# Optimization experiments

Hardware: AMD Instinct MI355X
Metric: run time of the kernel (lower is better)

## Reference

```python
import jax, jax.numpy as jnp
import numpy as np

N = 100000   # num_nodes
D = 128      # hidden_dim
E = 640000   # num_edges


def setup_inputs() -> dict:
    key = jax.random.key(0)
    k0, k1, k2, k3 = jax.random.split(key, 4)
    node_features = jax.random.normal(k0, (N, D), dtype=jnp.float32) * 0.02
    # GCNConv linear weights (glorot-style scale), bias initialized to zero
    scale = 1.0 / np.sqrt(D)
    W1 = jax.random.normal(k1, (D, D), dtype=jnp.float32) * scale
    b1 = jnp.zeros((D,), dtype=jnp.float32)
    W2 = jax.random.normal(k2, (D, D), dtype=jnp.float32) * scale
    b2 = jnp.zeros((D,), dtype=jnp.float32)
    edge_index = jax.random.randint(k3, (2, E), 0, N, dtype=jnp.int32)
    return {"node_features": node_features, "W1": W1, "b1": b1,
            "W2": W2, "b2": b2, "edge_index": edge_index}


def gcn_layer(x, W, b, row, col):
    # PyG GCNConv: linear (no bias) -> symmetric norm deg^-1/2 -> scatter-add -> +bias
    x = x @ W.T                                   # [N, D]
    ones = jnp.ones(row.shape, dtype=x.dtype)
    deg = jax.ops.segment_sum(ones, col, num_segments=N)   # in-degree incl. self-loops
    dis = jnp.where(deg > 0, jax.lax.rsqrt(deg), 0.0)       # deg_inv_sqrt, inf -> 0
    norm = dis[row] * dis[col]                    # [E_tot]
    msgs = norm[:, None] * x[row]                 # gather + scale, [E_tot, D]
    out = jax.ops.segment_sum(msgs, col, num_segments=N)    # scatter-aggregate
    return out + b


def reference(node_features, W1, b1, W2, b2, edge_index):
    # add self-loops once (GCNConv does this per call; same result since graph is static)
    loops = jnp.arange(N, dtype=edge_index.dtype)
    row = jnp.concatenate([edge_index[0], loops])
    col = jnp.concatenate([edge_index[1], loops])
    x = jax.nn.relu(gcn_layer(node_features, W1, b1, row, col))
    x = jax.nn.relu(gcn_layer(x, W2, b2, row, col))
    return x
```

## Files before the change

kernel.cpp:

```cpp
#include <hip/hip_runtime.h>

#define DD 128

typedef short bf16x8 __attribute__((ext_vector_type(8)));
typedef float f32x4 __attribute__((ext_vector_type(4)));

__device__ __forceinline__ unsigned short f2bf(float f) {
    unsigned int u = __builtin_bit_cast(unsigned int, f);
    u += 0x7fffu + ((u >> 16) & 1u);
    return (unsigned short)(u >> 16);
}
__device__ __forceinline__ float bflo(unsigned int u) { return __builtin_bit_cast(float, u << 16); }
__device__ __forceinline__ float bfhi(unsigned int u) { return __builtin_bit_cast(float, u & 0xffff0000u); }

__global__ __launch_bounds__(256) void k_part(const int* __restrict__ cnt,
                                              int* __restrict__ part, int n) {
    __shared__ int s[256];
    int t = threadIdx.x;
    int i = blockIdx.x * 256 + t;
    s[t] = (i < n) ? cnt[i] : 0;
    __syncthreads();
    for (int off = 128; off > 0; off >>= 1) {
        if (t < off) s[t] += s[t + off];
        __syncthreads();
    }
    if (t == 0) part[blockIdx.x] = s[0];
}

__global__ __launch_bounds__(1024) void k_scanpart(int* __restrict__ part, int nblk) {
    __shared__ int s[1024];
    int t = threadIdx.x;
    int v = (t < nblk) ? part[t] : 0;
    s[t] = v;
    __syncthreads();
    for (int off = 1; off < 1024; off <<= 1) {
        int u = (t >= off) ? s[t - off] : 0;
        __syncthreads();
        s[t] += u;
        __syncthreads();
    }
    if (t < nblk) part[t] = s[t] - v;
}

__global__ __launch_bounds__(256) void k_apply(const int* __restrict__ cnt,
                                               const int* __restrict__ part,
                                               int* __restrict__ rowptr,
                                               int* __restrict__ cursor,
                                               float* __restrict__ dis, int n) {
    __shared__ int s[256];
    int t = threadIdx.x;
    int i = blockIdx.x * 256 + t;
    int c = (i < n) ? cnt[i] : 0;
    s[t] = c;
    __syncthreads();
    for (int off = 1; off < 256; off <<= 1) {
        int u = (t >= off) ? s[t - off] : 0;
        __syncthreads();
        s[t] += u;
        __syncthreads();
    }
    int base = part[blockIdx.x] + s[t] - c;
    if (i < n) {
        rowptr[i] = base;
        cursor[i] = base;
        dis[i] = rsqrtf((float)c + 1.0f);
        if (i == n - 1) rowptr[n] = base + c;
    }
}

__global__ void k_permute(const int* __restrict__ row, const int* __restrict__ col,
                          int* __restrict__ cursor, int* __restrict__ srow, int E) {
    int e = blockIdx.x * blockDim.x + threadIdx.x;
    if (e >= E) return;
    int p = atomicAdd(&cursor[col[e]], 1);
    srow[p] = row[e];
}

__global__ __launch_bounds__(512) void k_gemm_mfma(const float* __restrict__ Xv,
                                                   const float* __restrict__ W,
                                                   unsigned short* __restrict__ Y,
                                                   int nrows, int gemm_blocks,
                                                   const int* __restrict__ ecol,
                                                   int* __restrict__ cnt, int E) {
    __shared__ unsigned short Ws[128 * 128];
    const int t = threadIdx.x;

    if ((int)blockIdx.x >= gemm_blocks) {
        int e = (blockIdx.x - gemm_blocks) * 512 + t;
        if (e < E) atomicAdd(&cnt[ecol[e]], 1);
        return;
    }

    #pragma unroll
    for (int i = 0; i < 4; ++i) {
        int g  = i * 512 + t;
        int wr = g >> 4, ch = g & 15;
        const float* src = W + wr * 128 + ch * 8;
        float4 f0 = *(const float4*)src;
        float4 f1 = *(const float4*)(src + 4);
        unsigned short u[8] = { f2bf(f0.x), f2bf(f0.y), f2bf(f0.z), f2bf(f0.w),
                                f2bf(f1.x), f2bf(f1.y), f2bf(f1.z), f2bf(f1.w) };
        int dst = wr * 128 + ((ch ^ (wr & 15)) << 3);
        *(uint4*)&Ws[dst] = *(const uint4*)u;
    }

    const int wid  = t >> 6;
    const int lane = t & 63;
    const int lr   = lane & 15;
    const int lk   = lane >> 4;
    const long base = (long)blockIdx.x * 128;

    long arow = base + wid * 16 + lr;
    bool rowok = arow < nrows;
    if (!rowok) arow = nrows - 1;

    float4 a[8];
    #pragma unroll
    for (int kc = 0; kc < 4; ++kc) {
        const float* ap = Xv + arow * 128 + kc * 32 + lk * 8;
        a[2 * kc]     = *(const float4*)ap;
        a[2 * kc + 1] = *(const float4*)(ap + 4);
    }
    __syncthreads();

    f32x4 acc[8] = {};
    #pragma unroll
    for (int kc = 0; kc < 4; ++kc) {
        bf16x8 af;
        af[0] = (short)f2bf(a[2*kc].x);   af[1] = (short)f2bf(a[2*kc].y);
        af[2] = (short)f2bf(a[2*kc].z);   af[3] = (short)f2bf(a[2*kc].w);
        af[4] = (short)f2bf(a[2*kc+1].x); af[5] = (short)f2bf(a[2*kc+1].y);
        af[6] = (short)f2bf(a[2*kc+1].z); af[7] = (short)f2bf(a[2*kc+1].w);
        #pragma unroll
        for (int jt = 0; jt < 8; ++jt) {
            int j  = jt * 16 + lr;
            int ch = (kc * 4 + lk) ^ lr;
            const bf16x8* bp = (const bf16x8*)&Ws[j * 128 + (ch << 3)];
            acc[jt] = __builtin_amdgcn_mfma_f32_16x16x32_bf16(*bp, af, acc[jt], 0, 0, 0);
        }
    }

    if (rowok) {
        unsigned short* yp = Y + arow * 128 + lk * 4;
        #pragma unroll
        for (int jt = 0; jt < 8; ++jt) {
            unsigned int d0 = (unsigned int)f2bf(acc[jt][0]) | ((unsigned int)f2bf(acc[jt][1]) << 16);
            unsigned int d1 = (unsigned int)f2bf(acc[jt][2]) | ((unsigned int)f2bf(acc[jt][3]) << 16);
            uint2 u; u.x = d0; u.y = d1;
            *(uint2*)(yp + jt * 16) = u;
        }
    }
}

__device__ __forceinline__ void fma8(float* acc, float nm, uint4 q) {
    acc[0] += nm * bflo(q.x); acc[1] += nm * bfhi(q.x);
    acc[2] += nm * bflo(q.y); acc[3] += nm * bfhi(q.y);
    acc[4] += nm * bflo(q.z); acc[5] += nm * bfhi(q.z);
    acc[6] += nm * bflo(q.w); acc[7] += nm * bfhi(q.w);
}

__device__ __forceinline__ void agg_node(const int* __restrict__ rowptr,
                                         const int* __restrict__ srow,
                                         const float* __restrict__ dis,
                                         const unsigned short* __restrict__ xw,
                                         const float* __restrict__ b,
                                         long v, int c, float* o) {
    float dv = dis[v], s = dv * dv;
    float acc[8] = {};
    fma8(acc, s, *(const uint4*)(xw + v * 128 + c));

    int e0 = rowptr[v], e1 = rowptr[v + 1];
    int nfull = (e1 - e0) >> 2;
    int e = e0;
    if (nfull) {
        int r0 = srow[e], r1 = srow[e + 1], r2 = srow[e + 2], r3 = srow[e + 3];
        for (int bi = 1; bi < nfull; ++bi) {
            int eb = e0 + bi * 4;
            int p0 = srow[eb], p1 = srow[eb + 1], p2 = srow[eb + 2], p3 = srow[eb + 3];
            float n0 = dis[r0] * dv, n1 = dis[r1] * dv;
            float n2 = dis[r2] * dv, n3 = dis[r3] * dv;
            uint4 q0 = *(const uint4*)(xw + (long)r0 * 128 + c);
            uint4 q1 = *(const uint4*)(xw + (long)r1 * 128 + c);
            uint4 q2 = *(const uint4*)(xw + (long)r2 * 128 + c);
            uint4 q3 = *(const uint4*)(xw + (long)r3 * 128 + c);
            fma8(acc, n0, q0); fma8(acc, n1, q1);
            fma8(acc, n2, q2); fma8(acc, n3, q3);
            r0 = p0; r1 = p1; r2 = p2; r3 = p3;
        }
        float n0 = dis[r0] * dv, n1 = dis[r1] * dv;
        float n2 = dis[r2] * dv, n3 = dis[r3] * dv;
        uint4 q0 = *(const uint4*)(xw + (long)r0 * 128 + c);
        uint4 q1 = *(const uint4*)(xw + (long)r1 * 128 + c);
        uint4 q2 = *(const uint4*)(xw + (long)r2 * 128 + c);
        uint4 q3 = *(const uint4*)(xw + (long)r3 * 128 + c);
        fma8(acc, n0, q0); fma8(acc, n1, q1);
        fma8(acc, n2, q2); fma8(acc, n3, q3);
        e = e0 + nfull * 4;
    }
    for (; e < e1; ++e) {
        int   r1 = srow[e];
        float n1 = dis[r1] * dv;
        fma8(acc, n1, *(const uint4*)(xw + (long)r1 * 128 + c));
    }

    float4 b0 = *(const float4*)(b + c);
    float4 b1 = *(const float4*)(b + c + 4);
    o[0] = fmaxf(acc[0] + b0.x, 0.0f); o[1] = fmaxf(acc[1] + b0.y, 0.0f);
    o[2] = fmaxf(acc[2] + b0.z, 0.0f); o[3] = fmaxf(acc[3] + b0.w, 0.0f);
    o[4] = fmaxf(acc[4] + b1.x, 0.0f); o[5] = fmaxf(acc[5] + b1.y, 0.0f);
    o[6] = fmaxf(acc[6] + b1.z, 0.0f); o[7] = fmaxf(acc[7] + b1.w, 0.0f);
}

__global__ __launch_bounds__(512) void k_agg_gemm(const int* __restrict__ rowptr,
                                                  const int* __restrict__ srow,
                                                  const float* __restrict__ dis,
                                                  const unsigned short* __restrict__ xw,
                                                  const float* __restrict__ b1,
                                                  const float* __restrict__ W2,
                                                  unsigned short* __restrict__ Y,
                                                  int n) {
    __shared__ unsigned short Ws[128 * 128];
    __shared__ unsigned short Hs[128 * 128];
    const int t = threadIdx.x;

    #pragma unroll
    for (int i = 0; i < 4; ++i) {
        int g  = i * 512 + t;
        int wr = g >> 4, ch = g & 15;
        const float* src = W2 + wr * 128 + ch * 8;
        float4 f0 = *(const float4*)src;
        float4 f1 = *(const float4*)(src + 4);
        unsigned short u[8] = { f2bf(f0.x), f2bf(f0.y), f2bf(f0.z), f2bf(f0.w),
                                f2bf(f1.x), f2bf(f1.y), f2bf(f1.z), f2bf(f1.w) };
        int dst = wr * 128 + ((ch ^ (wr & 15)) << 3);
        *(uint4*)&Ws[dst] = *(const uint4*)u;
    }

    const long nb = (long)blockIdx.x * 128;
    const int c  = (t & 15) * 8;
    #pragma unroll
    for (int pass = 0; pass < 4; ++pass) {
        int  lrow = pass * 32 + (t >> 4);
        long v    = nb + lrow;
        float o[8] = {};
        if (v < n) agg_node(rowptr, srow, dis, xw, b1, v, c, o);
        unsigned int pk[4];
        pk[0] = (unsigned int)f2bf(o[0]) | ((unsigned int)f2bf(o[1]) << 16);
        pk[1] = (unsigned int)f2bf(o[2]) | ((unsigned int)f2bf(o[3]) << 16);
        pk[2] = (unsigned int)f2bf(o[4]) | ((unsigned int)f2bf(o[5]) << 16);
        pk[3] = (unsigned int)f2bf(o[6]) | ((unsigned int)f2bf(o[7]) << 16);
        int ch = (t & 15) ^ (lrow & 15);
        *(uint4*)&Hs[lrow * 128 + (ch << 3)] = *(const uint4*)pk;
    }
    __syncthreads();

    const int wid  = t >> 6;
    const int lane = t & 63;
    const int lr   = lane & 15;
    const int lk   = lane >> 4;
    const int wrow = wid * 16 + lr;

    f32x4 acc[8] = {};
    #pragma unroll
    for (int kc = 0; kc < 4; ++kc) {
        int ach = (kc * 4 + lk) ^ (wrow & 15);
        bf16x8 af = *(const bf16x8*)&Hs[wrow * 128 + (ach << 3)];
        #pragma unroll
        for (int jt = 0; jt < 8; ++jt) {
            int j  = jt * 16 + lr;
            int ch = (kc * 4 + lk) ^ lr;
            const bf16x8* bp = (const bf16x8*)&Ws[j * 128 + (ch << 3)];
            acc[jt] = __builtin_amdgcn_mfma_f32_16x16x32_bf16(*bp, af, acc[jt], 0, 0, 0);
        }
    }

    long grow = nb + wrow;
    if (grow < n) {
        unsigned short* yp = Y + grow * 128 + lk * 4;
        #pragma unroll
        for (int jt = 0; jt < 8; ++jt) {
            unsigned int d0 = (unsigned int)f2bf(acc[jt][0]) | ((unsigned int)f2bf(acc[jt][1]) << 16);
            unsigned int d1 = (unsigned int)f2bf(acc[jt][2]) | ((unsigned int)f2bf(acc[jt][3]) << 16);
            uint2 u; u.x = d0; u.y = d1;
            *(uint2*)(yp + jt * 16) = u;
        }
    }
}

__global__ __launch_bounds__(256) void k_agg_out(const int* __restrict__ rowptr,
                                                 const int* __restrict__ srow,
                                                 const float* __restrict__ dis,
                                                 const unsigned short* __restrict__ xw,
                                                 const float* __restrict__ b,
                                                 float* __restrict__ out, int n) {
    long v = blockIdx.x * 16 + (threadIdx.x >> 4);
    if (v >= n) return;
    int c = (threadIdx.x & 15) * 8;
    float o[8];
    agg_node(rowptr, srow, dis, xw, b, v, c, o);
    float* op = out + v * 128 + c;
    *(float4*)op       = make_float4(o[0], o[1], o[2], o[3]);
    *(float4*)(op + 4) = make_float4(o[4], o[5], o[6], o[7]);
}

extern "C" void kernel_launch(void* const* d_in, const int* in_sizes, int n_in,
                              void* d_out, int out_size, void* d_ws, size_t ws_size,
                              hipStream_t stream) {
    const float* X  = (const float*)d_in[0];
    const float* W1 = (const float*)d_in[1];
    const float* b1 = (const float*)d_in[2];
    const float* W2 = (const float*)d_in[3];
    const float* b2 = (const float*)d_in[4];
    const int*   ei = (const int*)d_in[5];
    const int N = in_sizes[0] / DD;
    const int E = in_sizes[5] / 2;
    const int* row = ei;
    const int* col = ei + E;

    char* p = (char*)d_ws;
    auto carve = [&](size_t bytes) { char* q = p; p += (bytes + 255) & ~(size_t)255; return q; };
    int*            cnt    = (int*)           carve((size_t)N * 4);
    int*            rowptr = (int*)           carve((size_t)(N + 1) * 4);
    int*            cursor = (int*)           carve((size_t)N * 4);
    int*            part   = (int*)           carve(1024 * 4);
    int*            srow   = (int*)           carve((size_t)E * 4);
    float*          dis    = (float*)         carve((size_t)N * 4);
    unsigned short* xw     = (unsigned short*)carve((size_t)N * DD * 2);
    unsigned short* xw2    = (unsigned short*)carve((size_t)N * DD * 2);

    const int NBLK = (N + 255) / 256;
    const int gemm_grid = (N + 127) / 128;
    const int edge_grid = (E + 511) / 512;
    const int aggo_grid = (N + 15) / 16;

    hipMemsetAsync(cnt, 0, (size_t)N * 4, stream);
    k_gemm_mfma<<<gemm_grid + edge_grid, 512, 0, stream>>>(
        X, W1, xw, N, gemm_grid, col, cnt, E);

    k_part<<<NBLK, 256, 0, stream>>>(cnt, part, N);
    k_scanpart<<<1, 1024, 0, stream>>>(part, NBLK);
    k_apply<<<NBLK, 256, 0, stream>>>(cnt, part, rowptr, cursor, dis, N);
    k_permute<<<(E + 255) / 256, 256, 0, stream>>>(row, col, cursor, srow, E);

    k_agg_gemm<<<gemm_grid, 512, 0, stream>>>(rowptr, srow, dis, xw, b1, W2, xw2, N);

    k_agg_out<<<aggo_grid, 256, 0, stream>>>(rowptr, srow, dis, xw2, b2, (float*)d_out, N);
}
```

Measured before the change: 177.9 us.

## Fold block-prefix scan into apply kernel and halve agg-gemm tile rows

Removes the single-block k_scanpart launch: each k_apply block now sums all preceding partition totals itself, which saves a launch and a serial dependency at the cost of redundant reads (up to ~391 ints per block). The fused aggregate+GEMM kernel now processes 64 nodes per block instead of 128, with 8 waves split as 4 row tiles by 2 column halves. This doubles the grid and cuts shared memory per block, which should improve occupancy and load balance for the irregular gather, but W2 is converted and staged twice as often.

```diff
diff --git a/kernel.cpp b/kernel.cpp
--- a/kernel.cpp
+++ b/kernel.cpp
@@ -27,29 +27,28 @@
     if (t == 0) part[blockIdx.x] = s[0];
 }
 
-__global__ __launch_bounds__(1024) void k_scanpart(int* __restrict__ part, int nblk) {
-    __shared__ int s[1024];
-    int t = threadIdx.x;
-    int v = (t < nblk) ? part[t] : 0;
-    s[t] = v;
-    __syncthreads();
-    for (int off = 1; off < 1024; off <<= 1) {
-        int u = (t >= off) ? s[t - off] : 0;
-        __syncthreads();
-        s[t] += u;
-        __syncthreads();
-    }
-    if (t < nblk) part[t] = s[t] - v;
-}
-
 __global__ __launch_bounds__(256) void k_apply(const int* __restrict__ cnt,
                                                const int* __restrict__ part,
                                                int* __restrict__ rowptr,
                                                int* __restrict__ cursor,
                                                float* __restrict__ dis, int n) {
     __shared__ int s[256];
+    __shared__ int sbase;
     int t = threadIdx.x;
-    int i = blockIdx.x * 256 + t;
+    int bid = blockIdx.x;
+
+    int a = 0;
+    for (int j = t; j < bid; j += 256) a += part[j];
+    s[t] = a;
+    __syncthreads();
+    for (int off = 128; off > 0; off >>= 1) {
+        if (t < off) s[t] += s[t + off];
+        __syncthreads();
+    }
+    if (t == 0) sbase = s[0];
+    __syncthreads();
+
+    int i = bid * 256 + t;
     int c = (i < n) ? cnt[i] : 0;
     s[t] = c;
     __syncthreads();
@@ -59,7 +58,7 @@
         s[t] += u;
         __syncthreads();
     }
-    int base = part[blockIdx.x] + s[t] - c;
+    int base = sbase + s[t] - c;
     if (i < n) {
         rowptr[i] = base;
         cursor[i] = base;
@@ -220,7 +219,7 @@
                                                   unsigned short* __restrict__ Y,
                                                   int n) {
     __shared__ unsigned short Ws[128 * 128];
-    __shared__ unsigned short Hs[128 * 128];
+    __shared__ unsigned short Hs[64 * 128];
     const int t = threadIdx.x;
 
     #pragma unroll
@@ -236,10 +235,10 @@
         *(uint4*)&Ws[dst] = *(const uint4*)u;
     }
 
-    const long nb = (long)blockIdx.x * 128;
+    const long nb = (long)blockIdx.x * 64;
     const int c  = (t & 15) * 8;
     #pragma unroll
-    for (int pass = 0; pass < 4; ++pass) {
+    for (int pass = 0; pass < 2; ++pass) {
         int  lrow = pass * 32 + (t >> 4);
         long v    = nb + lrow;
         float o[8] = {};
@@ -258,19 +257,21 @@
     const int lane = t & 63;
     const int lr   = lane & 15;
     const int lk   = lane >> 4;
-    const int wrow = wid * 16 + lr;
-
-    f32x4 acc[8] = {};
+    const int rw   = wid & 3;
+    const int jb   = (wid >> 2) * 4;
+    const int wrow = rw * 16 + lr;
+
+    f32x4 acc[4] = {};
     #pragma unroll
     for (int kc = 0; kc < 4; ++kc) {
         int ach = (kc * 4 + lk) ^ (wrow & 15);
         bf16x8 af = *(const bf16x8*)&Hs[wrow * 128 + (ach << 3)];
         #pragma unroll
-        for (int jt = 0; jt < 8; ++jt) {
-            int j  = jt * 16 + lr;
+        for (int j4 = 0; j4 < 4; ++j4) {
+            int j  = (jb + j4) * 16 + lr;
             int ch = (kc * 4 + lk) ^ lr;
             const bf16x8* bp = (const bf16x8*)&Ws[j * 128 + (ch << 3)];
-            acc[jt] = __builtin_amdgcn_mfma_f32_16x16x32_bf16(*bp, af, acc[jt], 0, 0, 0);
+            acc[j4] = __builtin_amdgcn_mfma_f32_16x16x32_bf16(*bp, af, acc[j4], 0, 0, 0);
         }
     }
 
@@ -278,11 +279,11 @@
     if (grow < n) {
         unsigned short* yp = Y + grow * 128 + lk * 4;
         #pragma unroll
-        for (int jt = 0; jt < 8; ++jt) {
-            unsigned int d0 = (unsigned int)f2bf(acc[jt][0]) | ((unsigned int)f2bf(acc[jt][1]) << 16);
-            unsigned int d1 = (unsigned int)f2bf(acc[jt][2]) | ((unsigned int)f2bf(acc[jt][3]) << 16);
+        for (int j4 = 0; j4 < 4; ++j4) {
+            unsigned int d0 = (unsigned int)f2bf(acc[j4][0]) | ((unsigned int)f2bf(acc[j4][1]) << 16);
+            unsigned int d1 = (unsigned int)f2bf(acc[j4][2]) | ((unsigned int)f2bf(acc[j4][3]) << 16);
             uint2 u; u.x = d0; u.y = d1;
-            *(uint2*)(yp + jt * 16) = u;
+            *(uint2*)(yp + (jb + j4) * 16) = u;
         }
     }
 }
@@ -330,6 +331,7 @@
 
     const int NBLK = (N + 255) / 256;
     const int gemm_grid = (N + 127) / 128;
+    const int aggg_grid = (N + 63) / 64;
     const int edge_grid = (E + 511) / 512;
     const int aggo_grid = (N + 15) / 16;
 
@@ -338,11 +340,10 @@
         X, W1, xw, N, gemm_grid, col, cnt, E);
 
     k_part<<<NBLK, 256, 0, stream>>>(cnt, part, N);
-    k_scanpart<<<1, 1024, 0, stream>>>(part, NBLK);
     k_apply<<<NBLK, 256, 0, stream>>>(cnt, part, rowptr, cursor, dis, N);
     k_permute<<<(E + 255) / 256, 256, 0, stream>>>(row, col, cursor, srow, E);
 
-    k_agg_gemm<<<gemm_grid, 512, 0, stream>>>(rowptr, srow, dis, xw, b1, W2, xw2, N);
+    k_agg_gemm<<<aggg_grid, 512, 0, stream>>>(rowptr, srow, dis, xw, b1, W2, xw2, N);
 
     k_agg_out<<<aggo_grid, 256, 0, stream>>>(rowptr, srow, dis, xw2, b2, (float*)d_out, N);
 }
```

Result: faster. 170.4 us, median of 3 (-4.2%).
